# Kernel optimization log

Measured on AMD Instinct MI355X. Metric: run time of the kernel, lower is better.

The kernel has to match this reference:

```python
import jax, jax.numpy as jnp
import numpy as np

N, M = 1024, 32
FN, FE = 64, 32
AGG_N, AGG_E = 128, 64
OUT_N, OUT_E = 64, 32


def _build_indices(n, m):
    nip, eip = [], []
    k = 0
    for i in range(1, n):
        j0 = max(0, i - m)
        nip += list(range(j0, i))
        eip += list(range(k, k + i - j0))
        k += i - j0
    n1 = np.array(nip, np.int32)
    eT = np.array(eip, np.int32)
    n2 = np.concatenate([np.full(min(i, m), i, np.int32) for i in range(1, n)])
    # padded previous-node window indices (0 = zero pad slot)
    prev_nodes = np.zeros(n * m, np.int32)
    k = 0
    for i in range(n):
        t = min(i, m)
        prev_nodes[(i + 1) * m - t:(i + 1) * m] = np.arange(k, k + t) + 1
        k += t
    n_e = k
    norm_node = np.full(n, 1.0 / m, np.float32)
    for i in range(1, m):
        norm_node[i] = 1.0 / i
    prev_edges = np.zeros(n_e * m, np.int32)
    k = 0
    e = 0
    for i in range(n):
        j0 = max(0, i - m)
        for j in range(j0, i):
            if j > j0:
                prev_edges[(e + 1) * m - (j - j0):(e + 1) * m] = np.arange(k, k + j - j0) + 1
            e += 1
        k += i - j0
    norm_edge = np.ones(n_e, np.float32)
    k = 0
    for i in range(1, n):
        t = min(i, m)
        for j in range(t):
            if j > 0:
                norm_edge[k] = 1.0 / j
            k += 1
    return n1, eT, n2, prev_nodes, norm_node, prev_edges, norm_edge, n_e

N1, ET, N2, PREV_N, NORM_N, PREV_E, NORM_E, NE = _build_indices(N, M)
N1 = jnp.asarray(N1); ET = jnp.asarray(ET); N2 = jnp.asarray(N2)
PREV_N = jnp.asarray(PREV_N); PREV_E = jnp.asarray(PREV_E)
NORM_N = jnp.asarray(NORM_N); NORM_E = jnp.asarray(NORM_E)


def setup_inputs() -> dict:
    key = jax.random.key(0)
    ks = jax.random.split(key, 20)
    s = 0.02
    inp = {
        'input_nodes': jax.random.normal(ks[0], (2, N, FN), jnp.float32),
        'input_edges': jax.random.normal(ks[1], (2, NE, FE), jnp.float32),
        # node-branch MLPs (exclude_last=False)
        'Wan1': jax.random.normal(ks[2], (2 * FN + FE, 2 * AGG_N)) * s,
        'ban1': jnp.zeros((2 * AGG_N,)),
        'Wan2': jax.random.normal(ks[3], (2 * AGG_N, AGG_N)) * s,
        'ban2': jnp.zeros((AGG_N,)),
        'Wln1': jax.random.normal(ks[4], (AGG_N + FN, AGG_N + FN)) * s,
        'bln1': jnp.zeros((AGG_N + FN,)),
        'Wln2': jax.random.normal(ks[5], (AGG_N + FN, OUT_N)) * s,
        'bln2': jnp.zeros((OUT_N,)),
        # edge-branch MLPs
        'Wae1': jax.random.normal(ks[6], (FN + FE, 2 * AGG_E)) * s,
        'bae1': jnp.zeros((2 * AGG_E,)),
        'Wae2': jax.random.normal(ks[7], (2 * AGG_E, AGG_E)) * s,
        'bae2': jnp.zeros((AGG_E,)),
        'Wle1': jax.random.normal(ks[8], (AGG_E + FE, AGG_E + FE)) * s,
        'ble1': jnp.zeros((AGG_E + FE,)),
        'Wle2': jax.random.normal(ks[9], (AGG_E + FE, OUT_E)) * s,
        'ble2': jnp.zeros((OUT_E,)),
    }
    return inp


def _mlp2(x, W1, b1, W2, b2):
    return jax.nn.relu(jax.nn.relu(x @ W1 + b1) @ W2 + b2)


def reference(input_nodes, input_edges, Wan1, ban1, Wan2, ban2, Wln1, bln1, Wln2, bln2,
              Wae1, bae1, Wae2, bae2, Wle1, ble1, Wle2, ble2):
    B = input_nodes.shape[0]
    # gather node-edge pairs [B, NE, FN+FE] and node-edge-node triples [B, NE, 2FN+FE]
    pairs = jnp.concatenate([input_nodes[:, N1], input_edges[:, ET]], axis=-1)
    triples = jnp.concatenate([input_nodes[:, N1], input_edges[:, ET], input_nodes[:, N2]], axis=-1)
    # node branch (exclude_last=False -> triples)
    hn = _mlp2(triples, Wan1, ban1, Wan2, ban2)                     # [B, NE, AGG_N]
    hn = jnp.concatenate([jnp.zeros((B, 1, AGG_N), hn.dtype), hn], axis=1)
    pn = hn[:, PREV_N].reshape(B, N, M, AGG_N).sum(axis=2)          # padded window sum
    pn = pn * NORM_N[None, :, None]
    nodes_in = jnp.concatenate([pn, input_nodes], axis=-1)
    out_nodes = _mlp2(nodes_in, Wln1, bln1, Wln2, bln2)             # activation_nodes = relu
    # edge branch (pairs)
    he = _mlp2(pairs, Wae1, bae1, Wae2, bae2)                       # [B, NE, AGG_E]
    he = jnp.concatenate([jnp.zeros((B, 1, AGG_E), he.dtype), he], axis=1)
    pe = he[:, PREV_E].reshape(B, NE, M, AGG_E).sum(axis=2)
    pe = pe * NORM_E[None, :, None]
    edges_in = jnp.concatenate([pe, input_edges], axis=-1)
    out_edges = _mlp2(edges_in, Wle1, ble1, Wle2, ble2)             # activation_edges = relu
    return out_nodes, out_edges
```

## Files before the change

### kernel.cpp

```cpp
#include <hip/hip_runtime.h>
#include <cstdint>

#define NN    1024
#define MM    32
#define NEDGE 32240
#define MROWS 64480
#define PX    168
#define PST   392

typedef unsigned short ushort_t;

typedef __bf16 bf16x8 __attribute__((ext_vector_type(8)));
typedef float  floatx4 __attribute__((ext_vector_type(4)));

__device__ __forceinline__ float b2f(ushort_t u) {
    union { unsigned int i; float f; } v; v.i = ((unsigned int)u) << 16; return v.f;
}
__device__ __forceinline__ ushort_t f2b(float f) {
    unsigned int u = __builtin_bit_cast(unsigned int, f);
    u = (u + 0x7FFFu + ((u >> 16) & 1u)) >> 16;
    return (ushort_t)u;
}
__device__ __forceinline__ int edge_base(int i) {
    return (i <= MM) ? ((i * (i - 1)) >> 1) : (496 + (i - MM) * MM);
}
__device__ __forceinline__ void edge_ij(int e, int& i, int& j) {
    if (e < 496) {
        i = (int)((1.0f + sqrtf(8.0f * (float)e + 1.0f)) * 0.5f);
        while (((i * (i - 1)) >> 1) > e) --i;
        while (((i * (i + 1)) >> 1) <= e) ++i;
        j = e - ((i * (i - 1)) >> 1);
    } else {
        int q = e - 496;
        i = MM + (q >> 5);
        j = i - MM + (q & 31);
    }
}

__global__ __launch_bounds__(256) void k_pack(
        const float* an1, const float* an2, const float* ae1, const float* ae2,
        const float* le1, const float* le2, const float* ln1, const float* ln2,
        const float* nodes, const float* edges,
        ushort_t* pan1, ushort_t* pan2, ushort_t* pae1, ushort_t* pae2,
        ushort_t* ple1, ushort_t* ple2, ushort_t* pln1, ushort_t* pln2,
        ushort_t* nodesb, ushort_t* edgesb, int2* ijt) {
    __shared__ float tile[32][33];
    const int bid = blockIdx.x;
    const int tid = threadIdx.x;
    if (bid < 152) {
        const float* s; ushort_t* d; int K, N, t;
        if (bid < 40)       { s = an1; d = pan1; K = 160; N = 256; t = bid;       }
        else if (bid < 72)  { s = an2; d = pan2; K = 256; N = 128; t = bid - 40;  }
        else if (bid < 84)  { s = ae1; d = pae1; K = 96;  N = 128; t = bid - 72;  }
        else if (bid < 92)  { s = ae2; d = pae2; K = 128; N = 64;  t = bid - 84;  }
        else if (bid < 101) { s = le1; d = ple1; K = 96;  N = 96;  t = bid - 92;  }
        else if (bid < 104) { s = le2; d = ple2; K = 96;  N = 32;  t = bid - 101; }
        else if (bid < 140) { s = ln1; d = pln1; K = 192; N = 192; t = bid - 104; }
        else                { s = ln2; d = pln2; K = 192; N = 64;  t = bid - 140; }
        int ntn = N >> 5;
        int tk = t / ntn, tn = t - tk * ntn;
        int k0 = tk * 32, n0 = tn * 32;
        int tx = tid & 31, ty = tid >> 5;
#pragma unroll
        for (int m = 0; m < 4; ++m)
            tile[ty + m * 8][tx] = s[(size_t)(k0 + ty + m * 8) * N + n0 + tx];
        __syncthreads();
#pragma unroll
        for (int m = 0; m < 4; ++m)
            d[(size_t)(n0 + ty + m * 8) * K + k0 + tx] = f2b(tile[tx][ty + m * 8]);
    } else if (bid < 280) {
        int i4 = (bid - 152) * 256 + tid;
        float4 v = ((const float4*)nodes)[i4];
        uint2 o;
        o.x = (unsigned)f2b(v.x) | ((unsigned)f2b(v.y) << 16);
        o.y = (unsigned)f2b(v.z) | ((unsigned)f2b(v.w) << 16);
        ((uint2*)nodesb)[i4] = o;
    } else if (bid < 2296) {
        int i4 = (bid - 280) * 256 + tid;
        if (i4 < 515840) {
            float4 v = ((const float4*)edges)[i4];
            uint2 o;
            o.x = (unsigned)f2b(v.x) | ((unsigned)f2b(v.y) << 16);
            o.y = (unsigned)f2b(v.z) | ((unsigned)f2b(v.w) << 16);
            ((uint2*)edgesb)[i4] = o;
        }
    } else {
        int e = (bid - 2296) * 256 + tid;
        if (e < NEDGE) { int i, j; edge_ij(e, i, j); ijt[e] = make_int2(i, j); }
    }
}

__global__ __launch_bounds__(512, 2) void k_agg(
        const ushort_t* __restrict__ nodesb, const ushort_t* __restrict__ edgesb,
        const int2* __restrict__ ijt,
        const ushort_t* __restrict__ pan1, const float* __restrict__ ban1,
        const ushort_t* __restrict__ pan2, const float* __restrict__ ban2,
        const ushort_t* __restrict__ pae1, const float* __restrict__ bae1,
        const ushort_t* __restrict__ pae2, const float* __restrict__ bae2,
        ushort_t* __restrict__ hn, ushort_t* __restrict__ he) {
    __shared__ alignas(16) ushort_t X[32 * PX];
    __shared__ alignas(16) ushort_t H[32 * PST];
    __shared__ alignas(16) ushort_t SO[32 * 136];
    __shared__ alignas(16) ushort_t TO[32 * 72];
    const int tid = threadIdx.x;
    const int w = tid >> 6, l = tid & 63, lrow = l & 15, lq = l >> 4;
    const int mt = blockIdx.x;
    floatx4 zero = {0.f, 0.f, 0.f, 0.f};

    bf16x8 B0[5], B1[5], B2[3];
#pragma unroll
    for (int kt = 0; kt < 5; ++kt) {
        B0[kt] = *(const bf16x8*)(pan1 + (size_t)(16 * w + lrow) * 160 + kt * 32 + lq * 8);
        B1[kt] = *(const bf16x8*)(pan1 + (size_t)(16 * (w + 8) + lrow) * 160 + kt * 32 + lq * 8);
    }
#pragma unroll
    for (int kt = 0; kt < 3; ++kt)
        B2[kt] = *(const bf16x8*)(pae1 + (size_t)(16 * w + lrow) * 96 + kt * 32 + lq * 8);
    float c0 = ban1[16 * w + lrow];
    float c1 = ban1[16 * (w + 8) + lrow];
    float c2 = bae1[16 * w + lrow];

#pragma unroll
    for (int k = 0; k < 4; ++k) {
        int rr = w * 4 + k;
        int r = mt * 32 + rr;
        int off = (r >= NEDGE) ? 1 : 0;
        int2 ij = ijt[r - off * NEDGE];
        int bN = off * NN;
        unsigned* xr = (unsigned*)(X + rr * PX);
        const unsigned* nj = (const unsigned*)(nodesb + (size_t)(bN + ij.y) * 64);
        const unsigned* ni = (const unsigned*)(nodesb + (size_t)(bN + ij.x) * 64);
        const unsigned* eb = (const unsigned*)(edgesb + (size_t)r * 32);
        if (l < 32) { xr[l] = nj[l]; xr[48 + l] = ni[l]; }
        else        xr[l] = eb[l - 32];
    }
    __syncthreads();

#pragma unroll
    for (int s = 0; s < 2; ++s) {
        bf16x8 A[5];
#pragma unroll
        for (int kt = 0; kt < 5; ++kt)
            A[kt] = *(const bf16x8*)&X[(s * 16 + lrow) * PX + kt * 32 + lq * 8];
        floatx4 a0 = zero, a1 = zero, a2 = zero;
#pragma unroll
        for (int kt = 0; kt < 5; ++kt) {
            a0 = __builtin_amdgcn_mfma_f32_16x16x32_bf16(A[kt], B0[kt], a0, 0, 0, 0);
            a1 = __builtin_amdgcn_mfma_f32_16x16x32_bf16(A[kt], B1[kt], a1, 0, 0, 0);
        }
#pragma unroll
        for (int kt = 0; kt < 3; ++kt)
            a2 = __builtin_amdgcn_mfma_f32_16x16x32_bf16(A[kt], B2[kt], a2, 0, 0, 0);
#pragma unroll
        for (int r_ = 0; r_ < 4; ++r_) {
            int row = (s * 16 + lq * 4 + r_) * PST;
            H[row + 16 * w + lrow]       = f2b(fmaxf(a0[r_] + c0, 0.f));
            H[row + 128 + 16 * w + lrow] = f2b(fmaxf(a1[r_] + c1, 0.f));
            H[row + 256 + 16 * w + lrow] = f2b(fmaxf(a2[r_] + c2, 0.f));
        }
    }

    bf16x8 D0[8], D1[8], E[4];
    float d0 = 0.f, d1 = 0.f, d2 = 0.f;
    if (w < 4) {
#pragma unroll
        for (int kt = 0; kt < 8; ++kt) {
            D0[kt] = *(const bf16x8*)(pan2 + (size_t)(16 * w + lrow) * 256 + kt * 32 + lq * 8);
            D1[kt] = *(const bf16x8*)(pan2 + (size_t)(16 * (w + 4) + lrow) * 256 + kt * 32 + lq * 8);
        }
        d0 = ban2[16 * w + lrow];
        d1 = ban2[16 * (w + 4) + lrow];
    } else {
        int u = w - 4;
#pragma unroll
        for (int kt = 0; kt < 4; ++kt)
            E[kt] = *(const bf16x8*)(pae2 + (size_t)(16 * u + lrow) * 128 + kt * 32 + lq * 8);
        d2 = bae2[16 * u + lrow];
    }
    __syncthreads();

    if (w < 4) {
#pragma unroll
        for (int s = 0; s < 2; ++s) {
            floatx4 a0 = zero, a1 = zero;
#pragma unroll
            for (int kt = 0; kt < 8; ++kt) {
                bf16x8 a = *(const bf16x8*)&H[(s * 16 + lrow) * PST + kt * 32 + lq * 8];
                a0 = __builtin_amdgcn_mfma_f32_16x16x32_bf16(a, D0[kt], a0, 0, 0, 0);
                a1 = __builtin_amdgcn_mfma_f32_16x16x32_bf16(a, D1[kt], a1, 0, 0, 0);
            }
#pragma unroll
            for (int r_ = 0; r_ < 4; ++r_) {
                int row = (s * 16 + lq * 4 + r_) * 136;
                SO[row + 16 * w + lrow]      = f2b(fmaxf(a0[r_] + d0, 0.f));
                SO[row + 64 + 16 * w + lrow] = f2b(fmaxf(a1[r_] + d1, 0.f));
            }
        }
    } else {
        int u = w - 4;
#pragma unroll
        for (int s = 0; s < 2; ++s) {
            floatx4 a2 = zero;
#pragma unroll
            for (int kt = 0; kt < 4; ++kt) {
                bf16x8 a = *(const bf16x8*)&H[(s * 16 + lrow) * PST + 256 + kt * 32 + lq * 8];
                a2 = __builtin_amdgcn_mfma_f32_16x16x32_bf16(a, E[kt], a2, 0, 0, 0);
            }
#pragma unroll
            for (int r_ = 0; r_ < 4; ++r_)
                TO[(s * 16 + lq * 4 + r_) * 72 + 16 * u + lrow] = f2b(fmaxf(a2[r_] + d2, 0.f));
        }
    }
    __syncthreads();

    {
        int row = tid >> 4, c = tid & 15;
        ((uint4*)(hn + (size_t)(mt * 32 + row) * 128))[c] = *(const uint4*)&SO[row * 136 + c * 8];
        if (tid < 256) {
            int row2 = tid >> 3, c2 = tid & 7;
            ((uint4*)(he + (size_t)(mt * 32 + row2) * 64))[c2] = *(const uint4*)&TO[row2 * 72 + c2 * 8];
        }
    }
}

__global__ __launch_bounds__(256) void k_mid(
        const ushort_t* __restrict__ hn, const ushort_t* __restrict__ he,
        ushort_t* __restrict__ pn, ushort_t* __restrict__ pre) {
    const int tid = threadIdx.x;
    if (blockIdx.x < 2048) {
        int ri = blockIdx.x;
        int b = ri >> 10, i = ri & 1023;
        int t = min(i, MM);
        int base = b * NEDGE + edge_base(i);
        int c = tid & 63, g = tid >> 6;
        float s0 = 0.f, s1 = 0.f;
        for (int p = g; p < t; p += 4) {
            unsigned u = ((const unsigned*)(hn + (size_t)(base + p) * 128))[c];
            s0 += b2f((ushort_t)(u & 0xffff));
            s1 += b2f((ushort_t)(u >> 16));
        }
        __shared__ float red[4][128];
        red[g][c * 2] = s0; red[g][c * 2 + 1] = s1;
        __syncthreads();
        if (tid < 64) {
            float inv = 1.0f / (float)max(t, 1);
            float a0 = (red[0][tid * 2] + red[1][tid * 2] + red[2][tid * 2] + red[3][tid * 2]) * inv;
            float a1 = (red[0][tid * 2 + 1] + red[1][tid * 2 + 1] + red[2][tid * 2 + 1] + red[3][tid * 2 + 1]) * inv;
            ((unsigned*)(pn + (size_t)ri * 128))[tid] = (unsigned)f2b(a0) | ((unsigned)f2b(a1) << 16);
        }
    } else {
        int bi = blockIdx.x - 2048;
        int b = bi >> 10, i = bi & 1023;
        int t = min(i, MM);
        if (t == 0) return;
        int base = b * NEDGE + edge_base(i);
        __shared__ alignas(16) ushort_t hw[32 * 64];
        for (int u = tid; u < t * 8; u += 256)
            ((uint4*)hw)[u] = ((const uint4*)he)[(size_t)base * 8 + u];
        __syncthreads();
        if (tid < 64) {
            float run = 0.f;
            for (int p = 0; p < t; ++p) {
                float v = (p == 0) ? 0.f : run / (float)p;
                pre[(size_t)(base + p) * 64 + tid] = f2b(v);
                run += b2f(hw[p * 64 + tid]);
            }
        }
    }
}

__global__ __launch_bounds__(192) void k_final(
        const ushort_t* __restrict__ pn, const ushort_t* __restrict__ nodesb,
        const ushort_t* __restrict__ pln1, const float* __restrict__ bln1,
        const ushort_t* __restrict__ pln2, const float* __restrict__ bln2,
        float* __restrict__ out_nodes,
        const ushort_t* __restrict__ pre, const ushort_t* __restrict__ edgesb,
        const ushort_t* __restrict__ ple1, const float* __restrict__ ble1,
        const ushort_t* __restrict__ ple2, const float* __restrict__ ble2,
        float* __restrict__ out_edges) {
    __shared__ alignas(16) ushort_t LA[32 * 200];
    __shared__ alignas(16) ushort_t LB[32 * 200];
    const int tid = threadIdx.x;
    const int w = tid >> 6, l = tid & 63, lrow = l & 15, lq = l >> 4;
    floatx4 zero = {0.f, 0.f, 0.f, 0.f};

    if (blockIdx.x < 64) {
        int tile = blockIdx.x;
        for (int u = tid; u < 768; u += 192) {
            int row = u / 24, c = u - row * 24;
            int r = tile * 32 + row;
            const uint4* src = (c < 16) ? ((const uint4*)(pn + (size_t)r * 128) + c)
                                        : ((const uint4*)(nodesb + (size_t)r * 64) + (c - 16));
            *(uint4*)&LA[row * 200 + c * 8] = *src;
        }
        bf16x8 f1[6][4]; float v1[4];
#pragma unroll
        for (int kt = 0; kt < 6; ++kt)
#pragma unroll
            for (int nt = 0; nt < 4; ++nt)
                f1[kt][nt] = *(const bf16x8*)(pln1 + (size_t)(w * 64 + nt * 16 + lrow) * 192 + kt * 32 + lq * 8);
#pragma unroll
        for (int nt = 0; nt < 4; ++nt) v1[nt] = bln1[w * 64 + nt * 16 + lrow];
        __syncthreads();

        floatx4 acc[2][4];
#pragma unroll
        for (int s = 0; s < 2; ++s)
#pragma unroll
            for (int nt = 0; nt < 4; ++nt) acc[s][nt] = zero;
#pragma unroll
        for (int s = 0; s < 2; ++s)
#pragma unroll
            for (int kt = 0; kt < 6; ++kt) {
                bf16x8 a = *(const bf16x8*)&LA[(s * 16 + lrow) * 200 + kt * 32 + lq * 8];
#pragma unroll
                for (int nt = 0; nt < 4; ++nt)
                    acc[s][nt] = __builtin_amdgcn_mfma_f32_16x16x32_bf16(a, f1[kt][nt], acc[s][nt], 0, 0, 0);
            }
#pragma unroll
        for (int s = 0; s < 2; ++s)
#pragma unroll
            for (int nt = 0; nt < 4; ++nt) {
                int col = w * 64 + nt * 16 + lrow;
#pragma unroll
                for (int r_ = 0; r_ < 4; ++r_)
                    LB[(s * 16 + lq * 4 + r_) * 200 + col] = f2b(fmaxf(acc[s][nt][r_] + v1[nt], 0.f));
            }
        bf16x8 f2[6][2]; float v2[2] = {0.f, 0.f};
        if (w < 2) {
#pragma unroll
            for (int kt = 0; kt < 6; ++kt)
#pragma unroll
                for (int nt = 0; nt < 2; ++nt)
                    f2[kt][nt] = *(const bf16x8*)(pln2 + (size_t)(w * 32 + nt * 16 + lrow) * 192 + kt * 32 + lq * 8);
#pragma unroll
            for (int nt = 0; nt < 2; ++nt) v2[nt] = bln2[w * 32 + nt * 16 + lrow];
        }
        __syncthreads();
        if (w < 2) {
            floatx4 a2[2][2];
#pragma unroll
            for (int s = 0; s < 2; ++s) { a2[s][0] = zero; a2[s][1] = zero; }
#pragma unroll
            for (int s = 0; s < 2; ++s)
#pragma unroll
                for (int kt = 0; kt < 6; ++kt) {
                    bf16x8 a = *(const bf16x8*)&LB[(s * 16 + lrow) * 200 + kt * 32 + lq * 8];
#pragma unroll
                    for (int nt = 0; nt < 2; ++nt)
                        a2[s][nt] = __builtin_amdgcn_mfma_f32_16x16x32_bf16(a, f2[kt][nt], a2[s][nt], 0, 0, 0);
                }
#pragma unroll
            for (int s = 0; s < 2; ++s)
#pragma unroll
                for (int nt = 0; nt < 2; ++nt) {
                    int col = w * 32 + nt * 16 + lrow;
#pragma unroll
                    for (int r_ = 0; r_ < 4; ++r_)
                        out_nodes[(size_t)(tile * 32 + s * 16 + lq * 4 + r_) * 64 + col] =
                            fmaxf(a2[s][nt][r_] + v2[nt], 0.f);
                }
        }
    } else {
        int mt = blockIdx.x - 64;
        for (int u = tid; u < 384; u += 192) {
            int row = u / 12, c = u - row * 12;
            int r = mt * 32 + row;
            const uint4* src = (c < 8) ? ((const uint4*)(pre + (size_t)r * 64) + c)
                                       : ((const uint4*)(edgesb + (size_t)r * 32) + (c - 8));
            *(uint4*)&LA[row * 104 + c * 8] = *src;
        }
        bf16x8 fb1[3][2]; float v1[2];
#pragma unroll
        for (int kt = 0; kt < 3; ++kt)
#pragma unroll
            for (int nt = 0; nt < 2; ++nt)
                fb1[kt][nt] = *(const bf16x8*)(ple1 + (size_t)(w * 32 + nt * 16 + lrow) * 96 + kt * 32 + lq * 8);
#pragma unroll
        for (int nt = 0; nt < 2; ++nt) v1[nt] = ble1[w * 32 + nt * 16 + lrow];
        bf16x8 fb2[3]; float v2 = 0.f;
        if (w < 2) {
#pragma unroll
            for (int kt = 0; kt < 3; ++kt)
                fb2[kt] = *(const bf16x8*)(ple2 + (size_t)(w * 16 + lrow) * 96 + kt * 32 + lq * 8);
            v2 = ble2[w * 16 + lrow];
        }
        __syncthreads();

        floatx4 acc[2][2];
#pragma unroll
        for (int s = 0; s < 2; ++s) { acc[s][0] = zero; acc[s][1] = zero; }
#pragma unroll
        for (int s = 0; s < 2; ++s)
#pragma unroll
            for (int kt = 0; kt < 3; ++kt) {
                bf16x8 a = *(const bf16x8*)&LA[(s * 16 + lrow) * 104 + kt * 32 + lq * 8];
#pragma unroll
                for (int nt = 0; nt < 2; ++nt)
                    acc[s][nt] = __builtin_amdgcn_mfma_f32_16x16x32_bf16(a, fb1[kt][nt], acc[s][nt], 0, 0, 0);
            }
#pragma unroll
        for (int s = 0; s < 2; ++s)
#pragma unroll
            for (int nt = 0; nt < 2; ++nt) {
                int col = w * 32 + nt * 16 + lrow;
#pragma unroll
                for (int r_ = 0; r_ < 4; ++r_)
                    LB[(s * 16 + lq * 4 + r_) * 104 + col] = f2b(fmaxf(acc[s][nt][r_] + v1[nt], 0.f));
            }
        __syncthreads();
        if (w < 2) {
            floatx4 a2[2] = {zero, zero};
#pragma unroll
            for (int s = 0; s < 2; ++s)
#pragma unroll
                for (int kt = 0; kt < 3; ++kt) {
                    bf16x8 a = *(const bf16x8*)&LB[(s * 16 + lrow) * 104 + kt * 32 + lq * 8];
                    a2[s] = __builtin_amdgcn_mfma_f32_16x16x32_bf16(a, fb2[kt], a2[s], 0, 0, 0);
                }
#pragma unroll
            for (int s = 0; s < 2; ++s) {
                int col = w * 16 + lrow;
#pragma unroll
                for (int r_ = 0; r_ < 4; ++r_)
                    out_edges[(size_t)(mt * 32 + s * 16 + lq * 4 + r_) * 32 + col] = fmaxf(a2[s][r_] + v2, 0.f);
            }
        }
    }
}

extern "C" void kernel_launch(void* const* d_in, const int* in_sizes, int n_in,
                              void* d_out, int out_size, void* d_ws, size_t ws_size,
                              hipStream_t stream) {
    const float* nodes = (const float*)d_in[0];
    const float* edges = (const float*)d_in[1];
    const float* Wan1 = (const float*)d_in[2];  const float* ban1 = (const float*)d_in[3];
    const float* Wan2 = (const float*)d_in[4];  const float* ban2 = (const float*)d_in[5];
    const float* Wln1 = (const float*)d_in[6];  const float* bln1 = (const float*)d_in[7];
    const float* Wln2 = (const float*)d_in[8];  const float* bln2 = (const float*)d_in[9];
    const float* Wae1 = (const float*)d_in[10]; const float* bae1 = (const float*)d_in[11];
    const float* Wae2 = (const float*)d_in[12]; const float* bae2 = (const float*)d_in[13];
    const float* Wle1 = (const float*)d_in[14]; const float* ble1 = (const float*)d_in[15];
    const float* Wle2 = (const float*)d_in[16]; const float* ble2 = (const float*)d_in[17];

    char* ws = (char*)d_ws;
    size_t o = 0;
    auto alloc = [&](size_t bytes) -> void* {
        void* r = ws + o;
        o += (bytes + 255) & ~(size_t)255;
        return r;
    };
    ushort_t* hn     = (ushort_t*)alloc((size_t)MROWS * 128 * 2);
    ushort_t* he     = (ushort_t*)alloc((size_t)MROWS * 64 * 2);
    ushort_t* pre    = (ushort_t*)alloc((size_t)MROWS * 64 * 2);
    ushort_t* pn     = (ushort_t*)alloc((size_t)2048 * 128 * 2);
    ushort_t* nodesb = (ushort_t*)alloc((size_t)2 * NN * 64 * 2);
    ushort_t* edgesb = (ushort_t*)alloc((size_t)MROWS * 32 * 2);
    int2*     ijt    = (int2*)alloc((size_t)NEDGE * 8);
    ushort_t* pan1 = (ushort_t*)alloc(160 * 256 * 2);
    ushort_t* pan2 = (ushort_t*)alloc(256 * 128 * 2);
    ushort_t* pae1 = (ushort_t*)alloc(96 * 128 * 2);
    ushort_t* pae2 = (ushort_t*)alloc(128 * 64 * 2);
    ushort_t* ple1 = (ushort_t*)alloc(96 * 96 * 2);
    ushort_t* ple2 = (ushort_t*)alloc(96 * 32 * 2);
    ushort_t* pln1 = (ushort_t*)alloc(192 * 192 * 2);
    ushort_t* pln2 = (ushort_t*)alloc(192 * 64 * 2);

    float* out_nodes = (float*)d_out;
    float* out_edges = (float*)d_out + 2 * NN * 64;

    k_pack<<<2422, 256, 0, stream>>>(Wan1, Wan2, Wae1, Wae2, Wle1, Wle2, Wln1, Wln2,
                                     nodes, edges,
                                     pan1, pan2, pae1, pae2, ple1, ple2, pln1, pln2,
                                     nodesb, edgesb, ijt);
    k_agg<<<2015, 512, 0, stream>>>(nodesb, edgesb, ijt,
                                    pan1, ban1, pan2, ban2,
                                    pae1, bae1, pae2, bae2, hn, he);
    k_mid<<<4096, 256, 0, stream>>>(hn, he, pn, pre);
    k_final<<<64 + 2015, 192, 0, stream>>>(pn, nodesb, pln1, bln1, pln2, bln2, out_nodes,
                                           pre, edgesb, ple1, ble1, ple2, ble2, out_edges);

    (void)in_sizes; (void)n_in; (void)out_size; (void)ws_size;
}
```

Baseline: 165.5 us.

## Fuse four kernels into one persistent kernel with software grid barriers

Replaces the pack, aggregate, mid and final kernel launches with a single persistent kernel of 512 blocks that loops over tiles and separates the stages with atomic-counter grid barriers. The aim is to remove launch gaps and per-launch tail effects between the stages. In exchange it relies on all 512 blocks being co-resident (512 threads, up to 4 blocks per CU), adds barrier spin cost, and uses a magic-flag scheme with timeout breaks to reset the counters.

```diff
diff --git a/kernel.cpp b/kernel.cpp
--- a/kernel.cpp
+++ b/kernel.cpp
@@ -7,6 +7,8 @@
 #define MROWS 64480
 #define PX    168
 #define PST   392
+#define GRID  512
+#define MAGIC 0x13579BDFu
 
 typedef unsigned short ushort_t;
 
@@ -37,17 +39,55 @@
     }
 }
 
-__global__ __launch_bounds__(256) void k_pack(
-        const float* an1, const float* an2, const float* ae1, const float* ae2,
-        const float* le1, const float* le2, const float* ln1, const float* ln2,
-        const float* nodes, const float* edges,
+__device__ __forceinline__ void grid_barrier(unsigned* cnt, unsigned* flag) {
+    __syncthreads();
+    if (threadIdx.x == 0) {
+        if (flag) {
+            unsigned sp = 0;
+            while (__hip_atomic_load(flag, __ATOMIC_ACQUIRE, __HIP_MEMORY_SCOPE_AGENT) != MAGIC) {
+                __builtin_amdgcn_s_sleep(2);
+                if (++sp > 50000000u) break;
+            }
+        }
+        __threadfence();
+        __hip_atomic_fetch_add(cnt, 1u, __ATOMIC_ACQ_REL, __HIP_MEMORY_SCOPE_AGENT);
+        unsigned sp = 0;
+        while (__hip_atomic_load(cnt, __ATOMIC_ACQUIRE, __HIP_MEMORY_SCOPE_AGENT) < (unsigned)GRID) {
+            __builtin_amdgcn_s_sleep(2);
+            if (++sp > 50000000u) break;
+        }
+        __threadfence();
+    }
+    __syncthreads();
+}
+
+__global__ __launch_bounds__(512, 4) void k_mono(
+        const float* __restrict__ nodes, const float* __restrict__ edges,
+        const float* an1, const float* ban1, const float* an2, const float* ban2,
+        const float* ln1, const float* bln1, const float* ln2, const float* bln2,
+        const float* ae1, const float* bae1, const float* ae2, const float* bae2,
+        const float* le1, const float* ble1, const float* le2, const float* ble2,
+        unsigned* syncp,
         ushort_t* pan1, ushort_t* pan2, ushort_t* pae1, ushort_t* pae2,
         ushort_t* ple1, ushort_t* ple2, ushort_t* pln1, ushort_t* pln2,
-        ushort_t* nodesb, ushort_t* edgesb, int2* ijt) {
-    __shared__ float tile[32][33];
+        ushort_t* nodesb, ushort_t* edgesb, int2* ijt,
+        ushort_t* hn, ushort_t* he, ushort_t* pn, ushort_t* pre,
+        float* out_nodes, float* out_edges) {
+    __shared__ alignas(16) unsigned char arena[51200];
+    const int tid = threadIdx.x;
     const int bid = blockIdx.x;
-    const int tid = threadIdx.x;
+    floatx4 zero = {0.f, 0.f, 0.f, 0.f};
+    unsigned* flag = syncp;
+    unsigned* cnt  = syncp + 1;
+
+    if (bid == 0 && tid == 0) {
+        cnt[0] = 0; cnt[1] = 0; cnt[2] = 0;
+        __threadfence();
+        __hip_atomic_store(flag, MAGIC, __ATOMIC_RELEASE, __HIP_MEMORY_SCOPE_AGENT);
+    }
+
     if (bid < 152) {
+        float (*tile)[33] = (float(*)[33])arena;
         const float* s; ushort_t* d; int K, N, t;
         if (bid < 40)       { s = an1; d = pan1; K = 160; N = 256; t = bid;       }
         else if (bid < 72)  { s = an2; d = pan2; K = 256; N = 128; t = bid - 40;  }
@@ -62,368 +102,371 @@
         int k0 = tk * 32, n0 = tn * 32;
         int tx = tid & 31, ty = tid >> 5;
 #pragma unroll
-        for (int m = 0; m < 4; ++m)
-            tile[ty + m * 8][tx] = s[(size_t)(k0 + ty + m * 8) * N + n0 + tx];
+        for (int m = 0; m < 2; ++m)
+            tile[ty + m * 16][tx] = s[(size_t)(k0 + ty + m * 16) * N + n0 + tx];
         __syncthreads();
 #pragma unroll
-        for (int m = 0; m < 4; ++m)
-            d[(size_t)(n0 + ty + m * 8) * K + k0 + tx] = f2b(tile[tx][ty + m * 8]);
-    } else if (bid < 280) {
-        int i4 = (bid - 152) * 256 + tid;
-        float4 v = ((const float4*)nodes)[i4];
-        uint2 o;
-        o.x = (unsigned)f2b(v.x) | ((unsigned)f2b(v.y) << 16);
-        o.y = (unsigned)f2b(v.z) | ((unsigned)f2b(v.w) << 16);
-        ((uint2*)nodesb)[i4] = o;
-    } else if (bid < 2296) {
-        int i4 = (bid - 280) * 256 + tid;
-        if (i4 < 515840) {
+        for (int m = 0; m < 2; ++m)
+            d[(size_t)(n0 + ty + m * 16) * K + k0 + tx] = f2b(tile[tx][ty + m * 16]);
+    }
+    {
+        int idx = bid * 512 + tid;
+        if (idx < 32768) {
+            float4 v = ((const float4*)nodes)[idx];
+            uint2 o;
+            o.x = (unsigned)f2b(v.x) | ((unsigned)f2b(v.y) << 16);
+            o.y = (unsigned)f2b(v.z) | ((unsigned)f2b(v.w) << 16);
+            ((uint2*)nodesb)[idx] = o;
+        }
+        for (int i4 = idx; i4 < 515840; i4 += 262144) {
             float4 v = ((const float4*)edges)[i4];
             uint2 o;
             o.x = (unsigned)f2b(v.x) | ((unsigned)f2b(v.y) << 16);
             o.y = (unsigned)f2b(v.z) | ((unsigned)f2b(v.w) << 16);
             ((uint2*)edgesb)[i4] = o;
         }
-    } else {
-        int e = (bid - 2296) * 256 + tid;
-        if (e < NEDGE) { int i, j; edge_ij(e, i, j); ijt[e] = make_int2(i, j); }
-    }
-}
-
-__global__ __launch_bounds__(512, 2) void k_agg(
-        const ushort_t* __restrict__ nodesb, const ushort_t* __restrict__ edgesb,
-        const int2* __restrict__ ijt,
-        const ushort_t* __restrict__ pan1, const float* __restrict__ ban1,
-        const ushort_t* __restrict__ pan2, const float* __restrict__ ban2,
-        const ushort_t* __restrict__ pae1, const float* __restrict__ bae1,
-        const ushort_t* __restrict__ pae2, const float* __restrict__ bae2,
-        ushort_t* __restrict__ hn, ushort_t* __restrict__ he) {
-    __shared__ alignas(16) ushort_t X[32 * PX];
-    __shared__ alignas(16) ushort_t H[32 * PST];
-    __shared__ alignas(16) ushort_t SO[32 * 136];
-    __shared__ alignas(16) ushort_t TO[32 * 72];
-    const int tid = threadIdx.x;
-    const int w = tid >> 6, l = tid & 63, lrow = l & 15, lq = l >> 4;
-    const int mt = blockIdx.x;
-    floatx4 zero = {0.f, 0.f, 0.f, 0.f};
-
-    bf16x8 B0[5], B1[5], B2[3];
-#pragma unroll
-    for (int kt = 0; kt < 5; ++kt) {
-        B0[kt] = *(const bf16x8*)(pan1 + (size_t)(16 * w + lrow) * 160 + kt * 32 + lq * 8);
-        B1[kt] = *(const bf16x8*)(pan1 + (size_t)(16 * (w + 8) + lrow) * 160 + kt * 32 + lq * 8);
-    }
-#pragma unroll
-    for (int kt = 0; kt < 3; ++kt)
-        B2[kt] = *(const bf16x8*)(pae1 + (size_t)(16 * w + lrow) * 96 + kt * 32 + lq * 8);
-    float c0 = ban1[16 * w + lrow];
-    float c1 = ban1[16 * (w + 8) + lrow];
-    float c2 = bae1[16 * w + lrow];
-
-#pragma unroll
-    for (int k = 0; k < 4; ++k) {
-        int rr = w * 4 + k;
-        int r = mt * 32 + rr;
-        int off = (r >= NEDGE) ? 1 : 0;
-        int2 ij = ijt[r - off * NEDGE];
-        int bN = off * NN;
-        unsigned* xr = (unsigned*)(X + rr * PX);
-        const unsigned* nj = (const unsigned*)(nodesb + (size_t)(bN + ij.y) * 64);
-        const unsigned* ni = (const unsigned*)(nodesb + (size_t)(bN + ij.x) * 64);
-        const unsigned* eb = (const unsigned*)(edgesb + (size_t)r * 32);
-        if (l < 32) { xr[l] = nj[l]; xr[48 + l] = ni[l]; }
-        else        xr[l] = eb[l - 32];
-    }
-    __syncthreads();
-
-#pragma unroll
-    for (int s = 0; s < 2; ++s) {
-        bf16x8 A[5];
-#pragma unroll
-        for (int kt = 0; kt < 5; ++kt)
-            A[kt] = *(const bf16x8*)&X[(s * 16 + lrow) * PX + kt * 32 + lq * 8];
-        floatx4 a0 = zero, a1 = zero, a2 = zero;
-#pragma unroll
-        for (int kt = 0; kt < 5; ++kt) {
-            a0 = __builtin_amdgcn_mfma_f32_16x16x32_bf16(A[kt], B0[kt], a0, 0, 0, 0);
-            a1 = __builtin_amdgcn_mfma_f32_16x16x32_bf16(A[kt], B1[kt], a1, 0, 0, 0);
-        }
-#pragma unroll
-        for (int kt = 0; kt < 3; ++kt)
-            a2 = __builtin_amdgcn_mfma_f32_16x16x32_bf16(A[kt], B2[kt], a2, 0, 0, 0);
-#pragma unroll
-        for (int r_ = 0; r_ < 4; ++r_) {
-            int row = (s * 16 + lq * 4 + r_) * PST;
-            H[row + 16 * w + lrow]       = f2b(fmaxf(a0[r_] + c0, 0.f));
-            H[row + 128 + 16 * w + lrow] = f2b(fmaxf(a1[r_] + c1, 0.f));
-            H[row + 256 + 16 * w + lrow] = f2b(fmaxf(a2[r_] + c2, 0.f));
-        }
-    }
-
-    bf16x8 D0[8], D1[8], E[4];
-    float d0 = 0.f, d1 = 0.f, d2 = 0.f;
-    if (w < 4) {
-#pragma unroll
-        for (int kt = 0; kt < 8; ++kt) {
-            D0[kt] = *(const bf16x8*)(pan2 + (size_t)(16 * w + lrow) * 256 + kt * 32 + lq * 8);
-            D1[kt] = *(const bf16x8*)(pan2 + (size_t)(16 * (w + 4) + lrow) * 256 + kt * 32 + lq * 8);
-        }
-        d0 = ban2[16 * w + lrow];
-        d1 = ban2[16 * (w + 4) + lrow];
-    } else {
-        int u = w - 4;
-#pragma unroll
-        for (int kt = 0; kt < 4; ++kt)
-            E[kt] = *(const bf16x8*)(pae2 + (size_t)(16 * u + lrow) * 128 + kt * 32 + lq * 8);
-        d2 = bae2[16 * u + lrow];
-    }
-    __syncthreads();
-
-    if (w < 4) {
-#pragma unroll
-        for (int s = 0; s < 2; ++s) {
-            floatx4 a0 = zero, a1 = zero;
-#pragma unroll
-            for (int kt = 0; kt < 8; ++kt) {
-                bf16x8 a = *(const bf16x8*)&H[(s * 16 + lrow) * PST + kt * 32 + lq * 8];
-                a0 = __builtin_amdgcn_mfma_f32_16x16x32_bf16(a, D0[kt], a0, 0, 0, 0);
-                a1 = __builtin_amdgcn_mfma_f32_16x16x32_bf16(a, D1[kt], a1, 0, 0, 0);
-            }
-#pragma unroll
-            for (int r_ = 0; r_ < 4; ++r_) {
-                int row = (s * 16 + lq * 4 + r_) * 136;
-                SO[row + 16 * w + lrow]      = f2b(fmaxf(a0[r_] + d0, 0.f));
-                SO[row + 64 + 16 * w + lrow] = f2b(fmaxf(a1[r_] + d1, 0.f));
-            }
-        }
-    } else {
-        int u = w - 4;
-#pragma unroll
-        for (int s = 0; s < 2; ++s) {
-            floatx4 a2 = zero;
-#pragma unroll
-            for (int kt = 0; kt < 4; ++kt) {
-                bf16x8 a = *(const bf16x8*)&H[(s * 16 + lrow) * PST + 256 + kt * 32 + lq * 8];
-                a2 = __builtin_amdgcn_mfma_f32_16x16x32_bf16(a, E[kt], a2, 0, 0, 0);
-            }
-#pragma unroll
-            for (int r_ = 0; r_ < 4; ++r_)
-                TO[(s * 16 + lq * 4 + r_) * 72 + 16 * u + lrow] = f2b(fmaxf(a2[r_] + d2, 0.f));
-        }
-    }
-    __syncthreads();
+        if (idx < NEDGE) { int i, j; edge_ij(idx, i, j); ijt[idx] = make_int2(i, j); }
+    }
+    grid_barrier(&cnt[0], flag);
 
     {
-        int row = tid >> 4, c = tid & 15;
-        ((uint4*)(hn + (size_t)(mt * 32 + row) * 128))[c] = *(const uint4*)&SO[row * 136 + c * 8];
-        if (tid < 256) {
-            int row2 = tid >> 3, c2 = tid & 7;
-            ((uint4*)(he + (size_t)(mt * 32 + row2) * 64))[c2] = *(const uint4*)&TO[row2 * 72 + c2 * 8];
-        }
-    }
-}
-
-__global__ __launch_bounds__(256) void k_mid(
-        const ushort_t* __restrict__ hn, const ushort_t* __restrict__ he,
-        ushort_t* __restrict__ pn, ushort_t* __restrict__ pre) {
-    const int tid = threadIdx.x;
-    if (blockIdx.x < 2048) {
-        int ri = blockIdx.x;
-        int b = ri >> 10, i = ri & 1023;
-        int t = min(i, MM);
-        int base = b * NEDGE + edge_base(i);
-        int c = tid & 63, g = tid >> 6;
-        float s0 = 0.f, s1 = 0.f;
-        for (int p = g; p < t; p += 4) {
-            unsigned u = ((const unsigned*)(hn + (size_t)(base + p) * 128))[c];
-            s0 += b2f((ushort_t)(u & 0xffff));
-            s1 += b2f((ushort_t)(u >> 16));
-        }
-        __shared__ float red[4][128];
-        red[g][c * 2] = s0; red[g][c * 2 + 1] = s1;
-        __syncthreads();
-        if (tid < 64) {
-            float inv = 1.0f / (float)max(t, 1);
-            float a0 = (red[0][tid * 2] + red[1][tid * 2] + red[2][tid * 2] + red[3][tid * 2]) * inv;
-            float a1 = (red[0][tid * 2 + 1] + red[1][tid * 2 + 1] + red[2][tid * 2 + 1] + red[3][tid * 2 + 1]) * inv;
-            ((unsigned*)(pn + (size_t)ri * 128))[tid] = (unsigned)f2b(a0) | ((unsigned)f2b(a1) << 16);
-        }
-    } else {
-        int bi = blockIdx.x - 2048;
-        int b = bi >> 10, i = bi & 1023;
-        int t = min(i, MM);
-        if (t == 0) return;
-        int base = b * NEDGE + edge_base(i);
-        __shared__ alignas(16) ushort_t hw[32 * 64];
-        for (int u = tid; u < t * 8; u += 256)
-            ((uint4*)hw)[u] = ((const uint4*)he)[(size_t)base * 8 + u];
-        __syncthreads();
-        if (tid < 64) {
-            float run = 0.f;
-            for (int p = 0; p < t; ++p) {
-                float v = (p == 0) ? 0.f : run / (float)p;
-                pre[(size_t)(base + p) * 64 + tid] = f2b(v);
-                run += b2f(hw[p * 64 + tid]);
-            }
-        }
-    }
-}
-
-__global__ __launch_bounds__(192) void k_final(
-        const ushort_t* __restrict__ pn, const ushort_t* __restrict__ nodesb,
-        const ushort_t* __restrict__ pln1, const float* __restrict__ bln1,
-        const ushort_t* __restrict__ pln2, const float* __restrict__ bln2,
-        float* __restrict__ out_nodes,
-        const ushort_t* __restrict__ pre, const ushort_t* __restrict__ edgesb,
-        const ushort_t* __restrict__ ple1, const float* __restrict__ ble1,
-        const ushort_t* __restrict__ ple2, const float* __restrict__ ble2,
-        float* __restrict__ out_edges) {
-    __shared__ alignas(16) ushort_t LA[32 * 200];
-    __shared__ alignas(16) ushort_t LB[32 * 200];
-    const int tid = threadIdx.x;
-    const int w = tid >> 6, l = tid & 63, lrow = l & 15, lq = l >> 4;
-    floatx4 zero = {0.f, 0.f, 0.f, 0.f};
-
-    if (blockIdx.x < 64) {
-        int tile = blockIdx.x;
-        for (int u = tid; u < 768; u += 192) {
-            int row = u / 24, c = u - row * 24;
-            int r = tile * 32 + row;
-            const uint4* src = (c < 16) ? ((const uint4*)(pn + (size_t)r * 128) + c)
-                                        : ((const uint4*)(nodesb + (size_t)r * 64) + (c - 16));
-            *(uint4*)&LA[row * 200 + c * 8] = *src;
-        }
-        bf16x8 f1[6][4]; float v1[4];
-#pragma unroll
-        for (int kt = 0; kt < 6; ++kt)
-#pragma unroll
-            for (int nt = 0; nt < 4; ++nt)
-                f1[kt][nt] = *(const bf16x8*)(pln1 + (size_t)(w * 64 + nt * 16 + lrow) * 192 + kt * 32 + lq * 8);
-#pragma unroll
-        for (int nt = 0; nt < 4; ++nt) v1[nt] = bln1[w * 64 + nt * 16 + lrow];
-        __syncthreads();
-
-        floatx4 acc[2][4];
-#pragma unroll
-        for (int s = 0; s < 2; ++s)
-#pragma unroll
-            for (int nt = 0; nt < 4; ++nt) acc[s][nt] = zero;
-#pragma unroll
-        for (int s = 0; s < 2; ++s)
-#pragma unroll
-            for (int kt = 0; kt < 6; ++kt) {
-                bf16x8 a = *(const bf16x8*)&LA[(s * 16 + lrow) * 200 + kt * 32 + lq * 8];
-#pragma unroll
-                for (int nt = 0; nt < 4; ++nt)
-                    acc[s][nt] = __builtin_amdgcn_mfma_f32_16x16x32_bf16(a, f1[kt][nt], acc[s][nt], 0, 0, 0);
-            }
-#pragma unroll
-        for (int s = 0; s < 2; ++s)
-#pragma unroll
-            for (int nt = 0; nt < 4; ++nt) {
-                int col = w * 64 + nt * 16 + lrow;
-#pragma unroll
-                for (int r_ = 0; r_ < 4; ++r_)
-                    LB[(s * 16 + lq * 4 + r_) * 200 + col] = f2b(fmaxf(acc[s][nt][r_] + v1[nt], 0.f));
-            }
-        bf16x8 f2[6][2]; float v2[2] = {0.f, 0.f};
-        if (w < 2) {
-#pragma unroll
-            for (int kt = 0; kt < 6; ++kt)
-#pragma unroll
-                for (int nt = 0; nt < 2; ++nt)
-                    f2[kt][nt] = *(const bf16x8*)(pln2 + (size_t)(w * 32 + nt * 16 + lrow) * 192 + kt * 32 + lq * 8);
-#pragma unroll
-            for (int nt = 0; nt < 2; ++nt) v2[nt] = bln2[w * 32 + nt * 16 + lrow];
-        }
-        __syncthreads();
-        if (w < 2) {
-            floatx4 a2[2][2];
-#pragma unroll
-            for (int s = 0; s < 2; ++s) { a2[s][0] = zero; a2[s][1] = zero; }
-#pragma unroll
-            for (int s = 0; s < 2; ++s)
-#pragma unroll
-                for (int kt = 0; kt < 6; ++kt) {
-                    bf16x8 a = *(const bf16x8*)&LB[(s * 16 + lrow) * 200 + kt * 32 + lq * 8];
-#pragma unroll
-                    for (int nt = 0; nt < 2; ++nt)
-                        a2[s][nt] = __builtin_amdgcn_mfma_f32_16x16x32_bf16(a, f2[kt][nt], a2[s][nt], 0, 0, 0);
-                }
-#pragma unroll
-            for (int s = 0; s < 2; ++s)
-#pragma unroll
-                for (int nt = 0; nt < 2; ++nt) {
-                    int col = w * 32 + nt * 16 + lrow;
+        ushort_t* X  = (ushort_t*)arena;
+        ushort_t* H  = (ushort_t*)(arena + 10752);
+        ushort_t* SO = (ushort_t*)(arena + 35840);
+        ushort_t* TO = (ushort_t*)(arena + 44544);
+        const int w = tid >> 6, l = tid & 63, lrow = l & 15, lq = l >> 4;
+
+        for (int mt = bid; mt < 2015; mt += GRID) {
+            if (mt != bid) __syncthreads();
+
+            bf16x8 B0[5], B1[5], B2[3];
+#pragma unroll
+            for (int kt = 0; kt < 5; ++kt) {
+                B0[kt] = *(const bf16x8*)(pan1 + (size_t)(16 * w + lrow) * 160 + kt * 32 + lq * 8);
+                B1[kt] = *(const bf16x8*)(pan1 + (size_t)(16 * (w + 8) + lrow) * 160 + kt * 32 + lq * 8);
+            }
+#pragma unroll
+            for (int kt = 0; kt < 3; ++kt)
+                B2[kt] = *(const bf16x8*)(pae1 + (size_t)(16 * w + lrow) * 96 + kt * 32 + lq * 8);
+            float c0 = ban1[16 * w + lrow];
+            float c1 = ban1[16 * (w + 8) + lrow];
+            float c2 = bae1[16 * w + lrow];
+
+#pragma unroll
+            for (int k = 0; k < 4; ++k) {
+                int rr = w * 4 + k;
+                int r = mt * 32 + rr;
+                int off = (r >= NEDGE) ? 1 : 0;
+                int2 ij = ijt[r - off * NEDGE];
+                int bN = off * NN;
+                unsigned* xr = (unsigned*)(X + rr * PX);
+                const unsigned* nj = (const unsigned*)(nodesb + (size_t)(bN + ij.y) * 64);
+                const unsigned* ni = (const unsigned*)(nodesb + (size_t)(bN + ij.x) * 64);
+                const unsigned* eb = (const unsigned*)(edgesb + (size_t)r * 32);
+                if (l < 32) { xr[l] = nj[l]; xr[48 + l] = ni[l]; }
+                else        xr[l] = eb[l - 32];
+            }
+            __syncthreads();
+
+#pragma unroll
+            for (int s = 0; s < 2; ++s) {
+                bf16x8 A[5];
+#pragma unroll
+                for (int kt = 0; kt < 5; ++kt)
+                    A[kt] = *(const bf16x8*)&X[(s * 16 + lrow) * PX + kt * 32 + lq * 8];
+                floatx4 a0 = zero, a1 = zero, a2 = zero;
+#pragma unroll
+                for (int kt = 0; kt < 5; ++kt) {
+                    a0 = __builtin_amdgcn_mfma_f32_16x16x32_bf16(A[kt], B0[kt], a0, 0, 0, 0);
+                    a1 = __builtin_amdgcn_mfma_f32_16x16x32_bf16(A[kt], B1[kt], a1, 0, 0, 0);
+                }
+#pragma unroll
+                for (int kt = 0; kt < 3; ++kt)
+                    a2 = __builtin_amdgcn_mfma_f32_16x16x32_bf16(A[kt], B2[kt], a2, 0, 0, 0);
+#pragma unroll
+                for (int r_ = 0; r_ < 4; ++r_) {
+                    int row = (s * 16 + lq * 4 + r_) * PST;
+                    H[row + 16 * w + lrow]       = f2b(fmaxf(a0[r_] + c0, 0.f));
+                    H[row + 128 + 16 * w + lrow] = f2b(fmaxf(a1[r_] + c1, 0.f));
+                    H[row + 256 + 16 * w + lrow] = f2b(fmaxf(a2[r_] + c2, 0.f));
+                }
+            }
+
+            bf16x8 D0[8], D1[8], E[4];
+            float d0 = 0.f, d1 = 0.f, d2 = 0.f;
+            if (w < 4) {
+#pragma unroll
+                for (int kt = 0; kt < 8; ++kt) {
+                    D0[kt] = *(const bf16x8*)(pan2 + (size_t)(16 * w + lrow) * 256 + kt * 32 + lq * 8);
+                    D1[kt] = *(const bf16x8*)(pan2 + (size_t)(16 * (w + 4) + lrow) * 256 + kt * 32 + lq * 8);
+                }
+                d0 = ban2[16 * w + lrow];
+                d1 = ban2[16 * (w + 4) + lrow];
+            } else {
+                int u = w - 4;
+#pragma unroll
+                for (int kt = 0; kt < 4; ++kt)
+                    E[kt] = *(const bf16x8*)(pae2 + (size_t)(16 * u + lrow) * 128 + kt * 32 + lq * 8);
+                d2 = bae2[16 * u + lrow];
+            }
+            __syncthreads();
+
+            if (w < 4) {
+#pragma unroll
+                for (int s = 0; s < 2; ++s) {
+                    floatx4 a0 = zero, a1 = zero;
+#pragma unroll
+                    for (int kt = 0; kt < 8; ++kt) {
+                        bf16x8 a = *(const bf16x8*)&H[(s * 16 + lrow) * PST + kt * 32 + lq * 8];
+                        a0 = __builtin_amdgcn_mfma_f32_16x16x32_bf16(a, D0[kt], a0, 0, 0, 0);
+                        a1 = __builtin_amdgcn_mfma_f32_16x16x32_bf16(a, D1[kt], a1, 0, 0, 0);
+                    }
+#pragma unroll
+                    for (int r_ = 0; r_ < 4; ++r_) {
+                        int row = (s * 16 + lq * 4 + r_) * 136;
+                        SO[row + 16 * w + lrow]      = f2b(fmaxf(a0[r_] + d0, 0.f));
+                        SO[row + 64 + 16 * w + lrow] = f2b(fmaxf(a1[r_] + d1, 0.f));
+                    }
+                }
+            } else {
+                int u = w - 4;
+#pragma unroll
+                for (int s = 0; s < 2; ++s) {
+                    floatx4 a2 = zero;
+#pragma unroll
+                    for (int kt = 0; kt < 4; ++kt) {
+                        bf16x8 a = *(const bf16x8*)&H[(s * 16 + lrow) * PST + 256 + kt * 32 + lq * 8];
+                        a2 = __builtin_amdgcn_mfma_f32_16x16x32_bf16(a, E[kt], a2, 0, 0, 0);
+                    }
 #pragma unroll
                     for (int r_ = 0; r_ < 4; ++r_)
-                        out_nodes[(size_t)(tile * 32 + s * 16 + lq * 4 + r_) * 64 + col] =
-                            fmaxf(a2[s][nt][r_] + v2[nt], 0.f);
-                }
-        }
-    } else {
-        int mt = blockIdx.x - 64;
-        for (int u = tid; u < 384; u += 192) {
-            int row = u / 12, c = u - row * 12;
-            int r = mt * 32 + row;
-            const uint4* src = (c < 8) ? ((const uint4*)(pre + (size_t)r * 64) + c)
-                                       : ((const uint4*)(edgesb + (size_t)r * 32) + (c - 8));
-            *(uint4*)&LA[row * 104 + c * 8] = *src;
-        }
-        bf16x8 fb1[3][2]; float v1[2];
-#pragma unroll
-        for (int kt = 0; kt < 3; ++kt)
-#pragma unroll
-            for (int nt = 0; nt < 2; ++nt)
-                fb1[kt][nt] = *(const bf16x8*)(ple1 + (size_t)(w * 32 + nt * 16 + lrow) * 96 + kt * 32 + lq * 8);
-#pragma unroll
-        for (int nt = 0; nt < 2; ++nt) v1[nt] = ble1[w * 32 + nt * 16 + lrow];
-        bf16x8 fb2[3]; float v2 = 0.f;
-        if (w < 2) {
-#pragma unroll
-            for (int kt = 0; kt < 3; ++kt)
-                fb2[kt] = *(const bf16x8*)(ple2 + (size_t)(w * 16 + lrow) * 96 + kt * 32 + lq * 8);
-            v2 = ble2[w * 16 + lrow];
-        }
-        __syncthreads();
-
-        floatx4 acc[2][2];
-#pragma unroll
-        for (int s = 0; s < 2; ++s) { acc[s][0] = zero; acc[s][1] = zero; }
-#pragma unroll
-        for (int s = 0; s < 2; ++s)
-#pragma unroll
-            for (int kt = 0; kt < 3; ++kt) {
-                bf16x8 a = *(const bf16x8*)&LA[(s * 16 + lrow) * 104 + kt * 32 + lq * 8];
-#pragma unroll
-                for (int nt = 0; nt < 2; ++nt)
-                    acc[s][nt] = __builtin_amdgcn_mfma_f32_16x16x32_bf16(a, fb1[kt][nt], acc[s][nt], 0, 0, 0);
-            }
-#pragma unroll
-        for (int s = 0; s < 2; ++s)
-#pragma unroll
-            for (int nt = 0; nt < 2; ++nt) {
-                int col = w * 32 + nt * 16 + lrow;
-#pragma unroll
-                for (int r_ = 0; r_ < 4; ++r_)
-                    LB[(s * 16 + lq * 4 + r_) * 104 + col] = f2b(fmaxf(acc[s][nt][r_] + v1[nt], 0.f));
-            }
-        __syncthreads();
-        if (w < 2) {
-            floatx4 a2[2] = {zero, zero};
-#pragma unroll
-            for (int s = 0; s < 2; ++s)
-#pragma unroll
-                for (int kt = 0; kt < 3; ++kt) {
-                    bf16x8 a = *(const bf16x8*)&LB[(s * 16 + lrow) * 104 + kt * 32 + lq * 8];
-                    a2[s] = __builtin_amdgcn_mfma_f32_16x16x32_bf16(a, fb2[kt], a2[s], 0, 0, 0);
-                }
-#pragma unroll
-            for (int s = 0; s < 2; ++s) {
-                int col = w * 16 + lrow;
-#pragma unroll
-                for (int r_ = 0; r_ < 4; ++r_)
-                    out_edges[(size_t)(mt * 32 + s * 16 + lq * 4 + r_) * 32 + col] = fmaxf(a2[s][r_] + v2, 0.f);
+                        TO[(s * 16 + lq * 4 + r_) * 72 + 16 * u + lrow] = f2b(fmaxf(a2[r_] + d2, 0.f));
+                }
+            }
+            __syncthreads();
+
+            {
+                int row = tid >> 4, c = tid & 15;
+                ((uint4*)(hn + (size_t)(mt * 32 + row) * 128))[c] = *(const uint4*)&SO[row * 136 + c * 8];
+                if (tid < 256) {
+                    int row2 = tid >> 3, c2 = tid & 7;
+                    ((uint4*)(he + (size_t)(mt * 32 + row2) * 64))[c2] = *(const uint4*)&TO[row2 * 72 + c2 * 8];
+                }
+            }
+        }
+    }
+    grid_barrier(&cnt[1], nullptr);
+
+    {
+        const int half = tid >> 8, t5 = tid & 255;
+        for (int p = bid; p < 2048; p += GRID) {
+            if (p != bid) __syncthreads();
+            int item = 2 * p + half;
+            if (item < 2048) {
+                int ri = item;
+                int b = ri >> 10, i = ri & 1023;
+                int t = min(i, MM);
+                int base = b * NEDGE + edge_base(i);
+                int c = t5 & 63, g = t5 >> 6;
+                float s0 = 0.f, s1 = 0.f;
+                for (int q = g; q < t; q += 4) {
+                    unsigned u = ((const unsigned*)(hn + (size_t)(base + q) * 128))[c];
+                    s0 += b2f((ushort_t)(u & 0xffff));
+                    s1 += b2f((ushort_t)(u >> 16));
+                }
+                float* red = (float*)(arena + half * 4096);
+                red[g * 128 + c * 2] = s0; red[g * 128 + c * 2 + 1] = s1;
+                __syncthreads();
+                if (t5 < 64) {
+                    float inv = 1.0f / (float)max(t, 1);
+                    float a0 = (red[t5 * 2] + red[128 + t5 * 2] + red[256 + t5 * 2] + red[384 + t5 * 2]) * inv;
+                    float a1 = (red[t5 * 2 + 1] + red[128 + t5 * 2 + 1] + red[256 + t5 * 2 + 1] + red[384 + t5 * 2 + 1]) * inv;
+                    ((unsigned*)(pn + (size_t)ri * 128))[t5] = (unsigned)f2b(a0) | ((unsigned)f2b(a1) << 16);
+                }
+            } else {
+                int bi = item - 2048;
+                int b = bi >> 10, i = bi & 1023;
+                int t = min(i, MM);
+                int base = b * NEDGE + edge_base(i);
+                ushort_t* hw = (ushort_t*)(arena + half * 4096);
+                if (t > 0)
+                    for (int u = t5; u < t * 8; u += 256)
+                        ((uint4*)hw)[u] = ((const uint4*)he)[(size_t)base * 8 + u];
+                __syncthreads();
+                if (t > 0 && t5 < 64) {
+                    float run = 0.f;
+                    for (int q = 0; q < t; ++q) {
+                        float v = (q == 0) ? 0.f : run / (float)q;
+                        pre[(size_t)(base + q) * 64 + t5] = f2b(v);
+                        run += b2f(hw[q * 64 + t5]);
+                    }
+                }
+            }
+        }
+    }
+    grid_barrier(&cnt[2], nullptr);
+
+    {
+        const int half = tid >> 8, t8 = tid & 255;
+        const int w = t8 >> 6, l = t8 & 63, lrow = l & 15, lq = l >> 4;
+        unsigned char* hb = arena + half * 25600;
+        ushort_t* LA = (ushort_t*)hb;
+        ushort_t* LB = (ushort_t*)(hb + 12800);
+
+        for (int p = bid; p < 1040; p += GRID) {
+            if (p != bid) __syncthreads();
+            int item = 2 * p + half;
+            bool act = (t8 < 192) && (item < 2079);
+            if (item < 64) {
+                int tile = item;
+                if (act)
+                    for (int u = t8; u < 768; u += 192) {
+                        int row = u / 24, c = u - row * 24;
+                        int r = tile * 32 + row;
+                        const uint4* src = (c < 16) ? ((const uint4*)(pn + (size_t)r * 128) + c)
+                                                    : ((const uint4*)(nodesb + (size_t)r * 64) + (c - 16));
+                        *(uint4*)&LA[row * 200 + c * 8] = *src;
+                    }
+                bf16x8 f1[6][4]; float v1[4];
+                if (act) {
+#pragma unroll
+                    for (int kt = 0; kt < 6; ++kt)
+#pragma unroll
+                        for (int nt = 0; nt < 4; ++nt)
+                            f1[kt][nt] = *(const bf16x8*)(pln1 + (size_t)(w * 64 + nt * 16 + lrow) * 192 + kt * 32 + lq * 8);
+#pragma unroll
+                    for (int nt = 0; nt < 4; ++nt) v1[nt] = bln1[w * 64 + nt * 16 + lrow];
+                }
+                __syncthreads();
+                if (act) {
+                    floatx4 acc[2][4];
+#pragma unroll
+                    for (int s = 0; s < 2; ++s)
+#pragma unroll
+                        for (int nt = 0; nt < 4; ++nt) acc[s][nt] = zero;
+#pragma unroll
+                    for (int s = 0; s < 2; ++s)
+#pragma unroll
+                        for (int kt = 0; kt < 6; ++kt) {
+                            bf16x8 a = *(const bf16x8*)&LA[(s * 16 + lrow) * 200 + kt * 32 + lq * 8];
+#pragma unroll
+                            for (int nt = 0; nt < 4; ++nt)
+                                acc[s][nt] = __builtin_amdgcn_mfma_f32_16x16x32_bf16(a, f1[kt][nt], acc[s][nt], 0, 0, 0);
+                        }
+#pragma unroll
+                    for (int s = 0; s < 2; ++s)
+#pragma unroll
+                        for (int nt = 0; nt < 4; ++nt) {
+                            int col = w * 64 + nt * 16 + lrow;
+#pragma unroll
+                            for (int r_ = 0; r_ < 4; ++r_)
+                                LB[(s * 16 + lq * 4 + r_) * 200 + col] = f2b(fmaxf(acc[s][nt][r_] + v1[nt], 0.f));
+                        }
+                }
+                bf16x8 f2[6][2]; float v2[2] = {0.f, 0.f};
+                if (act && w < 2) {
+#pragma unroll
+                    for (int kt = 0; kt < 6; ++kt)
+#pragma unroll
+                        for (int nt = 0; nt < 2; ++nt)
+                            f2[kt][nt] = *(const bf16x8*)(pln2 + (size_t)(w * 32 + nt * 16 + lrow) * 192 + kt * 32 + lq * 8);
+#pragma unroll
+                    for (int nt = 0; nt < 2; ++nt) v2[nt] = bln2[w * 32 + nt * 16 + lrow];
+                }
+                __syncthreads();
+                if (act && w < 2) {
+                    floatx4 a2[2][2];
+#pragma unroll
+                    for (int s = 0; s < 2; ++s) { a2[s][0] = zero; a2[s][1] = zero; }
+#pragma unroll
+                    for (int s = 0; s < 2; ++s)
+#pragma unroll
+                        for (int kt = 0; kt < 6; ++kt) {
+                            bf16x8 a = *(const bf16x8*)&LB[(s * 16 + lrow) * 200 + kt * 32 + lq * 8];
+#pragma unroll
+                            for (int nt = 0; nt < 2; ++nt)
+                                a2[s][nt] = __builtin_amdgcn_mfma_f32_16x16x32_bf16(a, f2[kt][nt], a2[s][nt], 0, 0, 0);
+                        }
+#pragma unroll
+                    for (int s = 0; s < 2; ++s)
+#pragma unroll
+                        for (int nt = 0; nt < 2; ++nt) {
+                            int col = w * 32 + nt * 16 + lrow;
+#pragma unroll
+                            for (int r_ = 0; r_ < 4; ++r_)
+                                out_nodes[(size_t)(item * 32 + s * 16 + lq * 4 + r_) * 64 + col] =
+                                    fmaxf(a2[s][nt][r_] + v2[nt], 0.f);
+                        }
+                }
+            } else {
+                int mt = item - 64;
+                if (act)
+                    for (int u = t8; u < 384; u += 192) {
+                        int row = u / 12, c = u - row * 12;
+                        int r = mt * 32 + row;
+                        const uint4* src = (c < 8) ? ((const uint4*)(pre + (size_t)r * 64) + c)
+                                                   : ((const uint4*)(edgesb + (size_t)r * 32) + (c - 8));
+                        *(uint4*)&LA[row * 104 + c * 8] = *src;
+                    }
+                bf16x8 fb1[3][2]; float v1[2];
+                bf16x8 fb2[3]; float v2 = 0.f;
+                if (act) {
+#pragma unroll
+                    for (int kt = 0; kt < 3; ++kt)
+#pragma unroll
+                        for (int nt = 0; nt < 2; ++nt)
+                            fb1[kt][nt] = *(const bf16x8*)(ple1 + (size_t)(w * 32 + nt * 16 + lrow) * 96 + kt * 32 + lq * 8);
+#pragma unroll
+                    for (int nt = 0; nt < 2; ++nt) v1[nt] = ble1[w * 32 + nt * 16 + lrow];
+                    if (w < 2) {
+#pragma unroll
+                        for (int kt = 0; kt < 3; ++kt)
+                            fb2[kt] = *(const bf16x8*)(ple2 + (size_t)(w * 16 + lrow) * 96 + kt * 32 + lq * 8);
+                        v2 = ble2[w * 16 + lrow];
+                    }
+                }
+                __syncthreads();
+                if (act) {
+                    floatx4 acc[2][2];
+#pragma unroll
+                    for (int s = 0; s < 2; ++s) { acc[s][0] = zero; acc[s][1] = zero; }
+#pragma unroll
+                    for (int s = 0; s < 2; ++s)
+#pragma unroll
+                        for (int kt = 0; kt < 3; ++kt) {
+                            bf16x8 a = *(const bf16x8*)&LA[(s * 16 + lrow) * 104 + kt * 32 + lq * 8];
+#pragma unroll
+                            for (int nt = 0; nt < 2; ++nt)
+                                acc[s][nt] = __builtin_amdgcn_mfma_f32_16x16x32_bf16(a, fb1[kt][nt], acc[s][nt], 0, 0, 0);
+                        }
+#pragma unroll
+                    for (int s = 0; s < 2; ++s)
+#pragma unroll
+                        for (int nt = 0; nt < 2; ++nt) {
+                            int col = w * 32 + nt * 16 + lrow;
+#pragma unroll
+                            for (int r_ = 0; r_ < 4; ++r_)
+                                LB[(s * 16 + lq * 4 + r_) * 104 + col] = f2b(fmaxf(acc[s][nt][r_] + v1[nt], 0.f));
+                        }
+                }
+                __syncthreads();
+                if (act && w < 2) {
+                    floatx4 a2[2] = {zero, zero};
+#pragma unroll
+                    for (int s = 0; s < 2; ++s)
+#pragma unroll
+                        for (int kt = 0; kt < 3; ++kt) {
+                            bf16x8 a = *(const bf16x8*)&LB[(s * 16 + lrow) * 104 + kt * 32 + lq * 8];
+                            a2[s] = __builtin_amdgcn_mfma_f32_16x16x32_bf16(a, fb2[kt], a2[s], 0, 0, 0);
+                        }
+#pragma unroll
+                    for (int s = 0; s < 2; ++s) {
+                        int col = w * 16 + lrow;
+#pragma unroll
+                        for (int r_ = 0; r_ < 4; ++r_)
+                            out_edges[(size_t)(mt * 32 + s * 16 + lq * 4 + r_) * 32 + col] = fmaxf(a2[s][r_] + v2, 0.f);
+                    }
+                }
             }
         }
     }
@@ -450,6 +493,7 @@
         o += (bytes + 255) & ~(size_t)255;
         return r;
     };
+    unsigned* syncp  = (unsigned*)alloc(256);
     ushort_t* hn     = (ushort_t*)alloc((size_t)MROWS * 128 * 2);
     ushort_t* he     = (ushort_t*)alloc((size_t)MROWS * 64 * 2);
     ushort_t* pre    = (ushort_t*)alloc((size_t)MROWS * 64 * 2);
@@ -469,16 +513,13 @@
     float* out_nodes = (float*)d_out;
     float* out_edges = (float*)d_out + 2 * NN * 64;
 
-    k_pack<<<2422, 256, 0, stream>>>(Wan1, Wan2, Wae1, Wae2, Wle1, Wle2, Wln1, Wln2,
-                                     nodes, edges,
+    k_mono<<<GRID, 512, 0, stream>>>(nodes, edges,
+                                     Wan1, ban1, Wan2, ban2, Wln1, bln1, Wln2, bln2,
+                                     Wae1, bae1, Wae2, bae2, Wle1, ble1, Wle2, ble2,
+                                     syncp,
                                      pan1, pan2, pae1, pae2, ple1, ple2, pln1, pln2,
-                                     nodesb, edgesb, ijt);
-    k_agg<<<2015, 512, 0, stream>>>(nodesb, edgesb, ijt,
-                                    pan1, ban1, pan2, ban2,
-                                    pae1, bae1, pae2, bae2, hn, he);
-    k_mid<<<4096, 256, 0, stream>>>(hn, he, pn, pre);
-    k_final<<<64 + 2015, 192, 0, stream>>>(pn, nodesb, pln1, bln1, pln2, bln2, out_nodes,
-                                           pre, edgesb, ple1, ble1, ple2, ble2, out_edges);
+                                     nodesb, edgesb, ijt, hn, he, pn, pre,
+                                     out_nodes, out_edges);
 
     (void)in_sizes; (void)n_in; (void)out_size; (void)ws_size;
 }
```

Measured after the change: 513.7 us. 3.1x slower.
